# Performance work log

Measured on AMD Instinct MI355X. Metric: run time of the kernel, lower is better.

The kernel has to match this reference:

```python
import jax, jax.numpy as jnp
import numpy as np
import itertools

G = 80          # voxel grid side
N = 200000      # active voxels
A, B = 64, 128  # in/out channels
K = 27          # 3x3x3 kernel offsets
EPS = 1e-5


def _build_kernel_map():
    rng = np.random.default_rng(0)
    flat = rng.choice(G ** 3, size=N, replace=False)
    coords = np.stack(np.unravel_index(flat, (G, G, G)), axis=1).astype(np.int64)  # [N,3]
    lookup = np.full(G ** 3, -1, dtype=np.int64)
    lookup[flat] = np.arange(N)
    gidx = np.full((K, N), N, dtype=np.int32)  # pad with dummy row N
    sidx = np.full((K, N), N, dtype=np.int32)
    for k, off in enumerate(itertools.product([-1, 0, 1], repeat=3)):
        nb = coords + np.asarray(off)
        valid = np.all((nb >= 0) & (nb < G), axis=1)
        i_all = np.nonzero(valid)[0]
        nbf = np.ravel_multi_index(nb[valid].T, (G, G, G))
        j = lookup[nbf]
        m = j >= 0
        i, j = i_all[m], j[m]
        e = len(i)
        gidx[k, :e] = j   # gather neighbor features
        sidx[k, :e] = i   # scatter to output voxel
    return jnp.asarray(gidx), jnp.asarray(sidx)


def setup_inputs() -> dict:
    key = jax.random.key(0)
    ks = jax.random.split(key, 8)
    gidx, sidx = _build_kernel_map()
    return {
        "feats": jax.random.normal(ks[0], (N, A), jnp.float32),
        "w1": jax.random.normal(ks[1], (K, A, B), jnp.float32) * (1.0 / np.sqrt(K * A)),
        "w2": jax.random.normal(ks[2], (K, B, B), jnp.float32) * (1.0 / np.sqrt(K * B)),
        "w_nin": jax.random.normal(ks[3], (A, B), jnp.float32) * (1.0 / np.sqrt(A)),
        "bn1_gamma": jnp.ones((A,), jnp.float32),
        "bn1_beta": jnp.zeros((A,), jnp.float32),
        "bn2_gamma": jnp.ones((B,), jnp.float32),
        "bn2_beta": jnp.zeros((B,), jnp.float32),
        "gidx": gidx,
        "sidx": sidx,
    }


def _bn(x, gamma, beta):
    # MinkowskiBatchNorm: per-channel stats over all active voxels (training mode)
    mean = jnp.mean(x, axis=0)
    var = jnp.var(x, axis=0)
    return (x - mean) * jax.lax.rsqrt(var + EPS) * gamma + beta


def _sparse_conv(feats, w, gidx, sidx):
    # Minkowski sparse conv: for each kernel offset k, gather neighbor feats,
    # apply W[k], scatter-add to output voxel. Dummy row N absorbs padding.
    fp = jnp.concatenate([feats, jnp.zeros((1, feats.shape[1]), feats.dtype)], axis=0)
    out = jnp.zeros((N + 1, w.shape[-1]), feats.dtype)
    for k in range(w.shape[0]):  # fixed 27 offsets
        out = out.at[sidx[k]].add(fp[gidx[k]] @ w[k])
    return out[:N]


def reference(feats, w1, w2, w_nin, bn1_gamma, bn1_beta, bn2_gamma, bn2_beta, gidx, sidx):
    # resblock: BN(a) -> conv3(a->b) -> BN(b) -> conv3(b->b); skip via 1x1 conv (a!=b)
    h = _bn(feats, bn1_gamma, bn1_beta)
    h = _sparse_conv(h, w1, gidx, sidx)
    h = _bn(h, bn2_gamma, bn2_beta)
    residual = _sparse_conv(h, w2, gidx, sidx)
    skip = feats @ w_nin  # kernel_size=1 conv == per-voxel linear
    return skip + residual
```

## Files before the change

kernel.cpp:

```cpp
#include <hip/hip_runtime.h>

#define N_VOX 200000
#define NPAD_INV (27 * N_VOX + 128)
#define EPS_BN 1e-5f

typedef __bf16 bf16x8 __attribute__((ext_vector_type(8)));
typedef float f32x4 __attribute__((ext_vector_type(4)));

__device__ __forceinline__ float bf2f(unsigned short u) {
    union { float f; unsigned int i; } x; x.i = ((unsigned int)u) << 16; return x.f;
}
__device__ __forceinline__ unsigned short f2bf(float f) {
    union { float f; unsigned int i; } x; x.f = f;
    unsigned int r = x.i + 0x7fffu + ((x.i >> 16) & 1u);
    return (unsigned short)(r >> 16);
}

#define ASYNC16(gsrc, ldst)                                                             \
    __builtin_amdgcn_global_load_lds(                                                   \
        (const __attribute__((address_space(1))) void*)(gsrc),                          \
        (__attribute__((address_space(3))) void*)(ldst), 16, 0, 0)

__global__ void fill_inv_kernel(int* __restrict__ inv) {
    for (int i = blockIdx.x * 256 + threadIdx.x; i < NPAD_INV; i += gridDim.x * 256)
        inv[i] = N_VOX;
}

__global__ void build_inv_kernel(const int* __restrict__ sidx, const int* __restrict__ gidx,
                                 int* __restrict__ inv) {
    int k = blockIdx.y;
    int p = blockIdx.x * 256 + threadIdx.x;
    if (p < N_VOX) {
        int s = sidx[k * N_VOX + p];
        if (s < N_VOX) inv[k * N_VOX + s] = gidx[k * N_VOX + p];
    }
}

__global__ void tr_w1_kernel(const float* __restrict__ w, unsigned short* __restrict__ wt) {
    int k = blockIdx.y; int idx = blockIdx.x * 256 + threadIdx.x;
    int a = idx >> 7, b = idx & 127;
    wt[k * 8192 + b * 64 + a] = f2bf(w[k * 8192 + idx]);
}
__global__ void tr_w2_kernel(const float* __restrict__ w, unsigned short* __restrict__ wt) {
    int k = blockIdx.y; int idx = blockIdx.x * 256 + threadIdx.x;
    int a = idx >> 7, b = idx & 127;
    wt[k * 16384 + b * 128 + a] = f2bf(w[k * 16384 + idx]);
}
__global__ void tr_wn_kernel(const float* __restrict__ w, unsigned short* __restrict__ wt) {
    int idx = blockIdx.x * 256 + threadIdx.x;
    int a = idx >> 7, b = idx & 127;
    wt[b * 64 + a] = f2bf(w[idx]);
}

__global__ void stats1_kernel(const float* __restrict__ feats,
                              float* __restrict__ sum, float* __restrict__ sq) {
    int t = threadIdx.x; int c = t & 63; int rg = t >> 6;
    float s = 0.f, q = 0.f;
    for (int row = blockIdx.x * 4 + rg; row < N_VOX; row += gridDim.x * 4) {
        float x = feats[(size_t)row * 64 + c];
        s += x; q += x * x;
    }
    __shared__ float red[8][64];
    red[rg][c] = s; red[4 + rg][c] = q;
    __syncthreads();
    if (t < 64) atomicAdd(&sum[t], red[0][t] + red[1][t] + red[2][t] + red[3][t]);
    else if (t < 128) { int cc = t - 64; atomicAdd(&sq[cc], red[4][cc] + red[5][cc] + red[6][cc] + red[7][cc]); }
}

__global__ void stats2_kernel(const unsigned short* __restrict__ h1b,
                              float* __restrict__ sum, float* __restrict__ sq) {
    int t = threadIdx.x; int c = t & 127; int rg = t >> 7;
    float s = 0.f, q = 0.f;
    for (int row = blockIdx.x * 2 + rg; row < N_VOX; row += gridDim.x * 2) {
        float x = bf2f(h1b[(size_t)row * 128 + c]);
        s += x; q += x * x;
    }
    __shared__ float red[4][128];
    red[rg][c] = s; red[2 + rg][c] = q;
    __syncthreads();
    if (t < 128) atomicAdd(&sum[t], red[0][t] + red[1][t]);
    else { int cc = t - 128; atomicAdd(&sq[cc], red[2][cc] + red[3][cc]); }
}

__global__ void norm1_kernel(const float* __restrict__ feats, const float* __restrict__ ssum,
                             const float* __restrict__ ssq, const float* __restrict__ gamma,
                             const float* __restrict__ beta, unsigned short* __restrict__ fA,
                             unsigned short* __restrict__ fRaw) {
    __shared__ float sc[64], sh[64];
    int t = threadIdx.x;
    if (t < 64) {
        float mean = ssum[t] * (1.0f / N_VOX);
        float var  = ssq[t] * (1.0f / N_VOX) - mean * mean;
        float s    = gamma[t] * rsqrtf(var + EPS_BN);
        sc[t] = s; sh[t] = beta[t] - mean * s;
    }
    __syncthreads();
    const int total = N_VOX * 64 / 8;
    int i = blockIdx.x * 256 + t;
    if (i >= total) return;
    int cb = (i * 8) & 63;
    const float4* src = (const float4*)(feats + (size_t)i * 8);
    float4 f0 = src[0], f1 = src[1];
    float fv[8] = {f0.x, f0.y, f0.z, f0.w, f1.x, f1.y, f1.z, f1.w};
    union { uint4 q; unsigned short u[8]; } a, r;
#pragma unroll
    for (int j = 0; j < 8; j++) {
        a.u[j] = f2bf(fv[j] * sc[cb + j] + sh[cb + j]);
        r.u[j] = f2bf(fv[j]);
    }
    *(uint4*)(fA + (size_t)i * 8) = a.q;
    *(uint4*)(fRaw + (size_t)i * 8) = r.q;
}

__global__ void norm2_kernel(unsigned short* __restrict__ h1b, const float* __restrict__ ssum,
                             const float* __restrict__ ssq, const float* __restrict__ gamma,
                             const float* __restrict__ beta) {
    __shared__ float sc[128], sh[128];
    int t = threadIdx.x;
    if (t < 128) {
        float mean = ssum[t] * (1.0f / N_VOX);
        float var  = ssq[t] * (1.0f / N_VOX) - mean * mean;
        float s    = gamma[t] * rsqrtf(var + EPS_BN);
        sc[t] = s; sh[t] = beta[t] - mean * s;
    }
    __syncthreads();
    const int total = N_VOX * 128 / 8;
    int i = blockIdx.x * 256 + t;
    if (i >= total) return;
    int cb = (i * 8) & 127;
    union { uint4 q; unsigned short u[8]; } v;
    v.q = *(const uint4*)(h1b + (size_t)i * 8);
#pragma unroll
    for (int j = 0; j < 8; j++) v.u[j] = f2bf(bf2f(v.u[j]) * sc[cb + j] + sh[cb + j]);
    *(uint4*)(h1b + (size_t)i * 8) = v.q;
}

__global__ __launch_bounds__(256) void conv1_kernel(
    const unsigned short* __restrict__ fA, const unsigned short* __restrict__ w1t,
    const int* __restrict__ inv, const unsigned short* __restrict__ zp,
    unsigned short* __restrict__ h1b) {
    __shared__ __align__(16) unsigned short sA[2][128 * 64];
    __shared__ __align__(16) unsigned short sB[2][128 * 64];
    const int t = threadIdx.x, lane = t & 63, w = t >> 6;
    const int v0 = blockIdx.x * 128;
    const int srow = w * 32;
    const int lrow = lane >> 3;
    const int lcol = (lane & 7) * 8;
    const int scol = lcol ^ (lrow * 8);
    const int m0 = (w & 1) * 64, n0 = (w >> 1) * 64;
    const int l16 = lane & 15, quad = lane >> 4;
    const int xs = l16 & 7;
    f32x4 acc[4][4] = {};

    auto stage = [&](int k, int b) {
#pragma unroll
        for (int q = 0; q < 4; q++) {
            int rt = srow + q * 8 + lrow;
            int g = inv[k * N_VOX + v0 + rt];
            const unsigned short* asrc = (g < N_VOX) ? (fA + (size_t)g * 64 + scol) : (zp + scol);
            ASYNC16(asrc, &sA[b][(srow + q * 8) * 64]);
            const unsigned short* bsrc = w1t + k * 8192 + rt * 64 + scol;
            ASYNC16(bsrc, &sB[b][(srow + q * 8) * 64]);
        }
    };

    stage(0, 0);
    for (int j = 0; j < 27; j++) {
        const int cb = j & 1;
        if (j + 1 < 27) {
            stage(j + 1, cb ^ 1);
            asm volatile("s_waitcnt vmcnt(8)" ::: "memory");
        } else {
            asm volatile("s_waitcnt vmcnt(0)" ::: "memory");
        }
        __builtin_amdgcn_sched_barrier(0);
        __builtin_amdgcn_s_barrier();
        __builtin_amdgcn_sched_barrier(0);
#pragma unroll
        for (int ks = 0; ks < 2; ks++) {
            const int cs = ((ks * 4 + quad) ^ xs) * 8;
            bf16x8 af[4], bfr[4];
#pragma unroll
            for (int mi = 0; mi < 4; mi++)
                af[mi] = *(const bf16x8*)&sA[cb][(m0 + mi * 16 + l16) * 64 + cs];
#pragma unroll
            for (int ni = 0; ni < 4; ni++)
                bfr[ni] = *(const bf16x8*)&sB[cb][(n0 + ni * 16 + l16) * 64 + cs];
            __builtin_amdgcn_s_setprio(1);
#pragma unroll
            for (int mi = 0; mi < 4; mi++)
#pragma unroll
                for (int ni = 0; ni < 4; ni++)
                    acc[mi][ni] = __builtin_amdgcn_mfma_f32_16x16x32_bf16(af[mi], bfr[ni], acc[mi][ni], 0, 0, 0);
            __builtin_amdgcn_s_setprio(0);
        }
        __builtin_amdgcn_sched_barrier(0);
        __builtin_amdgcn_s_barrier();
        __builtin_amdgcn_sched_barrier(0);
    }
#pragma unroll
    for (int mi = 0; mi < 4; mi++)
#pragma unroll
        for (int r = 0; r < 4; r++) {
            int v = v0 + m0 + mi * 16 + quad * 4 + r;
            if (v < N_VOX) {
#pragma unroll
                for (int ni = 0; ni < 4; ni++)
                    h1b[(size_t)v * 128 + n0 + ni * 16 + l16] = f2bf(acc[mi][ni][r]);
            }
        }
}

__global__ __launch_bounds__(256) void conv2_kernel(
    const unsigned short* __restrict__ h1n, const unsigned short* __restrict__ fRaw,
    const unsigned short* __restrict__ w2t, const unsigned short* __restrict__ w_nint,
    const int* __restrict__ inv, const unsigned short* __restrict__ zp,
    float* __restrict__ out) {
    __shared__ __align__(16) unsigned short sA[2][128 * 64];
    __shared__ __align__(16) unsigned short sB[2][128 * 64];
    const int t = threadIdx.x, lane = t & 63, w = t >> 6;
    const int v0 = blockIdx.x * 128;
    const int srow = w * 32;
    const int lrow = lane >> 3;
    const int lcol = (lane & 7) * 8;
    const int scol = lcol ^ (lrow * 8);
    const int m0 = (w & 1) * 64, n0 = (w >> 1) * 64;
    const int l16 = lane & 15, quad = lane >> 4;
    const int xs = l16 & 7;
    f32x4 acc[4][4] = {};

    auto stage = [&](int j, int b) {
        if (j < 54) {
            const int ko = j >> 1;
            const int kh = (j & 1) * 64;
#pragma unroll
            for (int q = 0; q < 4; q++) {
                int rt = srow + q * 8 + lrow;
                int g = inv[ko * N_VOX + v0 + rt];
                const unsigned short* asrc = (g < N_VOX) ? (h1n + (size_t)g * 128 + kh + scol) : (zp + scol);
                ASYNC16(asrc, &sA[b][(srow + q * 8) * 64]);
                const unsigned short* bsrc = w2t + ko * 16384 + rt * 128 + kh + scol;
                ASYNC16(bsrc, &sB[b][(srow + q * 8) * 64]);
            }
        } else {
#pragma unroll
            for (int q = 0; q < 4; q++) {
                int rt = srow + q * 8 + lrow;
                int v = v0 + rt;
                const unsigned short* asrc = (v < N_VOX) ? (fRaw + (size_t)v * 64 + scol) : (zp + scol);
                ASYNC16(asrc, &sA[b][(srow + q * 8) * 64]);
                const unsigned short* bsrc = w_nint + rt * 64 + scol;
                ASYNC16(bsrc, &sB[b][(srow + q * 8) * 64]);
            }
        }
    };

    stage(0, 0);
    for (int jj = 0; jj < 55; jj++) {
        const int cb = jj & 1;
        if (jj + 1 < 55) {
            stage(jj + 1, cb ^ 1);
            asm volatile("s_waitcnt vmcnt(8)" ::: "memory");
        } else {
            asm volatile("s_waitcnt vmcnt(0)" ::: "memory");
        }
        __builtin_amdgcn_sched_barrier(0);
        __builtin_amdgcn_s_barrier();
        __builtin_amdgcn_sched_barrier(0);
#pragma unroll
        for (int ks = 0; ks < 2; ks++) {
            const int cs = ((ks * 4 + quad) ^ xs) * 8;
            bf16x8 af[4], bfr[4];
#pragma unroll
            for (int mi = 0; mi < 4; mi++)
                af[mi] = *(const bf16x8*)&sA[cb][(m0 + mi * 16 + l16) * 64 + cs];
#pragma unroll
            for (int ni = 0; ni < 4; ni++)
                bfr[ni] = *(const bf16x8*)&sB[cb][(n0 + ni * 16 + l16) * 64 + cs];
            __builtin_amdgcn_s_setprio(1);
#pragma unroll
            for (int mi = 0; mi < 4; mi++)
#pragma unroll
                for (int ni = 0; ni < 4; ni++)
                    acc[mi][ni] = __builtin_amdgcn_mfma_f32_16x16x32_bf16(af[mi], bfr[ni], acc[mi][ni], 0, 0, 0);
            __builtin_amdgcn_s_setprio(0);
        }
        __builtin_amdgcn_sched_barrier(0);
        __builtin_amdgcn_s_barrier();
        __builtin_amdgcn_sched_barrier(0);
    }
#pragma unroll
    for (int mi = 0; mi < 4; mi++)
#pragma unroll
        for (int r = 0; r < 4; r++) {
            int v = v0 + m0 + mi * 16 + quad * 4 + r;
            if (v < N_VOX) {
#pragma unroll
                for (int ni = 0; ni < 4; ni++)
                    out[(size_t)v * 128 + n0 + ni * 16 + l16] = acc[mi][ni][r];
            }
        }
}

extern "C" void kernel_launch(void* const* d_in, const int* in_sizes, int n_in,
                              void* d_out, int out_size, void* d_ws, size_t ws_size,
                              hipStream_t stream) {
    const float* feats = (const float*)d_in[0];
    const float* w1    = (const float*)d_in[1];
    const float* w2    = (const float*)d_in[2];
    const float* w_nin = (const float*)d_in[3];
    const float* g1    = (const float*)d_in[4];
    const float* b1    = (const float*)d_in[5];
    const float* g2    = (const float*)d_in[6];
    const float* b2    = (const float*)d_in[7];
    const int* gidx = (const int*)d_in[8];
    const int* sidx = (const int*)d_in[9];
    float* out = (float*)d_out;

    char* ws = (char*)d_ws;
    int* inv               = (int*)(ws);
    unsigned short* fA     = (unsigned short*)(ws + 21600512);
    unsigned short* fRaw   = (unsigned short*)(ws + 47200512);
    unsigned short* h1b    = (unsigned short*)(ws + 72800512);
    unsigned short* w1t    = (unsigned short*)(ws + 124000512);
    unsigned short* w2t    = (unsigned short*)(ws + 124442880);
    unsigned short* w_nint = (unsigned short*)(ws + 125327616);
    float* stats           = (float*)(ws + 125344000);
    unsigned short* zp     = (unsigned short*)(ws + 125345536);
    float* s1sum = stats, *s1sq = stats + 64, *s2sum = stats + 128, *s2sq = stats + 256;

    hipMemsetAsync(stats, 0, 1536 + 256, stream);
    fill_inv_kernel<<<2048, 256, 0, stream>>>(inv);
    build_inv_kernel<<<dim3(782, 27), 256, 0, stream>>>(sidx, gidx, inv);
    tr_w1_kernel<<<dim3(32, 27), 256, 0, stream>>>(w1, w1t);
    tr_w2_kernel<<<dim3(64, 27), 256, 0, stream>>>(w2, w2t);
    tr_wn_kernel<<<32, 256, 0, stream>>>(w_nin, w_nint);
    stats1_kernel<<<512, 256, 0, stream>>>(feats, s1sum, s1sq);
    norm1_kernel<<<6250, 256, 0, stream>>>(feats, s1sum, s1sq, g1, b1, fA, fRaw);
    conv1_kernel<<<1563, 256, 0, stream>>>(fA, w1t, inv, zp, h1b);
    stats2_kernel<<<512, 256, 0, stream>>>(h1b, s2sum, s2sq);
    norm2_kernel<<<12500, 256, 0, stream>>>(h1b, s2sum, s2sq, g2, b2);
    conv2_kernel<<<1563, 256, 0, stream>>>(h1b, fRaw, w2t, w_nint, inv, zp, out);
}
```

Before: 757.1 us.

## Fold batch-norm affine into conv weights and fuse stats into conv epilogue

Batch-norm scale is folded into the transposed conv weights, and the shift becomes a per-offset bias term. That bias is added per output row only for the kernel offsets that have a valid neighbor, tracked with a shared-memory presence bitmask. This removes the separate normalize passes over the activations and the fA buffer. The second BN's statistics are accumulated in the conv1 epilogue, and the raw-feature conversion, input stats and inv fill are merged into a single prep kernel. The trade-off is extra atomics and bias work in the conv kernels, and slightly different bf16 rounding because the scale is applied to the weights instead of the activations.

Measured after the change: 1.345 ms. +77.7%, slower.

```diff
diff --git a/kernel.cpp b/kernel.cpp
--- a/kernel.cpp
+++ b/kernel.cpp
@@ -21,9 +21,49 @@
         (const __attribute__((address_space(1))) void*)(gsrc),                          \
         (__attribute__((address_space(3))) void*)(ldst), 16, 0, 0)
 
-__global__ void fill_inv_kernel(int* __restrict__ inv) {
-    for (int i = blockIdx.x * 256 + threadIdx.x; i < NPAD_INV; i += gridDim.x * 256)
-        inv[i] = N_VOX;
+__global__ void prep0_kernel(const float* __restrict__ feats, const float* __restrict__ w_nin,
+                             int* __restrict__ inv, unsigned short* __restrict__ w_nint,
+                             unsigned short* __restrict__ fRaw,
+                             float* __restrict__ s1sum, float* __restrict__ s1sq) {
+    __shared__ float rs[64], rq[64];
+    const int t = threadIdx.x;
+    if (t < 64) { rs[t] = 0.f; rq[t] = 0.f; }
+    __syncthreads();
+    const int stride = gridDim.x * 256;
+    for (int i = blockIdx.x * 256 + t; i < NPAD_INV; i += stride) inv[i] = N_VOX;
+    for (int i = blockIdx.x * 256 + t; i < 8192; i += stride) {
+        int a = i >> 7, b = i & 127;
+        w_nint[b * 64 + a] = f2bf(w_nin[i]);
+    }
+    float s[8] = {}, q[8] = {};
+    const int total = N_VOX * 64 / 8;
+    for (int i = blockIdx.x * 256 + t; i < total; i += stride) {
+        const float4* src = (const float4*)(feats + (size_t)i * 8);
+        float4 f0 = src[0], f1 = src[1];
+        float fv[8] = {f0.x, f0.y, f0.z, f0.w, f1.x, f1.y, f1.z, f1.w};
+        union { uint4 u4; unsigned short u[8]; } r;
+#pragma unroll
+        for (int j = 0; j < 8; j++) {
+            r.u[j] = f2bf(fv[j]);
+            s[j] += fv[j]; q[j] += fv[j] * fv[j];
+        }
+        *(uint4*)(fRaw + (size_t)i * 8) = r.u4;
+    }
+#pragma unroll
+    for (int j = 0; j < 8; j++) {
+        s[j] += __shfl_xor(s[j], 8, 64); s[j] += __shfl_xor(s[j], 16, 64); s[j] += __shfl_xor(s[j], 32, 64);
+        q[j] += __shfl_xor(q[j], 8, 64); q[j] += __shfl_xor(q[j], 16, 64); q[j] += __shfl_xor(q[j], 32, 64);
+    }
+    const int lane = t & 63;
+    if (lane < 8) {
+#pragma unroll
+        for (int j = 0; j < 8; j++) {
+            atomicAdd(&rs[lane * 8 + j], s[j]);
+            atomicAdd(&rq[lane * 8 + j], q[j]);
+        }
+    }
+    __syncthreads();
+    if (t < 64) { atomicAdd(&s1sum[t], rs[t]); atomicAdd(&s1sq[t], rq[t]); }
 }
 
 __global__ void build_inv_kernel(const int* __restrict__ sidx, const int* __restrict__ gidx,
@@ -36,111 +76,71 @@
     }
 }
 
-__global__ void tr_w1_kernel(const float* __restrict__ w, unsigned short* __restrict__ wt) {
-    int k = blockIdx.y; int idx = blockIdx.x * 256 + threadIdx.x;
-    int a = idx >> 7, b = idx & 127;
-    wt[k * 8192 + b * 64 + a] = f2bf(w[k * 8192 + idx]);
-}
-__global__ void tr_w2_kernel(const float* __restrict__ w, unsigned short* __restrict__ wt) {
-    int k = blockIdx.y; int idx = blockIdx.x * 256 + threadIdx.x;
-    int a = idx >> 7, b = idx & 127;
-    wt[k * 16384 + b * 128 + a] = f2bf(w[k * 16384 + idx]);
-}
-__global__ void tr_wn_kernel(const float* __restrict__ w, unsigned short* __restrict__ wt) {
-    int idx = blockIdx.x * 256 + threadIdx.x;
-    int a = idx >> 7, b = idx & 127;
-    wt[b * 64 + a] = f2bf(w[idx]);
-}
-
-__global__ void stats1_kernel(const float* __restrict__ feats,
-                              float* __restrict__ sum, float* __restrict__ sq) {
-    int t = threadIdx.x; int c = t & 63; int rg = t >> 6;
-    float s = 0.f, q = 0.f;
-    for (int row = blockIdx.x * 4 + rg; row < N_VOX; row += gridDim.x * 4) {
-        float x = feats[(size_t)row * 64 + c];
-        s += x; q += x * x;
-    }
-    __shared__ float red[8][64];
-    red[rg][c] = s; red[4 + rg][c] = q;
-    __syncthreads();
-    if (t < 64) atomicAdd(&sum[t], red[0][t] + red[1][t] + red[2][t] + red[3][t]);
-    else if (t < 128) { int cc = t - 64; atomicAdd(&sq[cc], red[4][cc] + red[5][cc] + red[6][cc] + red[7][cc]); }
-}
-
-__global__ void stats2_kernel(const unsigned short* __restrict__ h1b,
-                              float* __restrict__ sum, float* __restrict__ sq) {
-    int t = threadIdx.x; int c = t & 127; int rg = t >> 7;
-    float s = 0.f, q = 0.f;
-    for (int row = blockIdx.x * 2 + rg; row < N_VOX; row += gridDim.x * 2) {
-        float x = bf2f(h1b[(size_t)row * 128 + c]);
-        s += x; q += x * x;
-    }
-    __shared__ float red[4][128];
-    red[rg][c] = s; red[2 + rg][c] = q;
-    __syncthreads();
-    if (t < 128) atomicAdd(&sum[t], red[0][t] + red[1][t]);
-    else { int cc = t - 128; atomicAdd(&sq[cc], red[2][cc] + red[3][cc]); }
-}
-
-__global__ void norm1_kernel(const float* __restrict__ feats, const float* __restrict__ ssum,
-                             const float* __restrict__ ssq, const float* __restrict__ gamma,
-                             const float* __restrict__ beta, unsigned short* __restrict__ fA,
-                             unsigned short* __restrict__ fRaw) {
-    __shared__ float sc[64], sh[64];
-    int t = threadIdx.x;
+__global__ void prep1_kernel(const float* __restrict__ w1, const float* __restrict__ s1sum,
+                             const float* __restrict__ s1sq, const float* __restrict__ g1,
+                             const float* __restrict__ b1, unsigned short* __restrict__ w1t,
+                             float* __restrict__ T1g) {
+    __shared__ float lsc[64], lsh[64];
+    const int t = threadIdx.x;
     if (t < 64) {
-        float mean = ssum[t] * (1.0f / N_VOX);
-        float var  = ssq[t] * (1.0f / N_VOX) - mean * mean;
-        float s    = gamma[t] * rsqrtf(var + EPS_BN);
-        sc[t] = s; sh[t] = beta[t] - mean * s;
-    }
-    __syncthreads();
-    const int total = N_VOX * 64 / 8;
-    int i = blockIdx.x * 256 + t;
-    if (i >= total) return;
-    int cb = (i * 8) & 63;
-    const float4* src = (const float4*)(feats + (size_t)i * 8);
-    float4 f0 = src[0], f1 = src[1];
-    float fv[8] = {f0.x, f0.y, f0.z, f0.w, f1.x, f1.y, f1.z, f1.w};
-    union { uint4 q; unsigned short u[8]; } a, r;
-#pragma unroll
-    for (int j = 0; j < 8; j++) {
-        a.u[j] = f2bf(fv[j] * sc[cb + j] + sh[cb + j]);
-        r.u[j] = f2bf(fv[j]);
-    }
-    *(uint4*)(fA + (size_t)i * 8) = a.q;
-    *(uint4*)(fRaw + (size_t)i * 8) = r.q;
-}
-
-__global__ void norm2_kernel(unsigned short* __restrict__ h1b, const float* __restrict__ ssum,
-                             const float* __restrict__ ssq, const float* __restrict__ gamma,
-                             const float* __restrict__ beta) {
-    __shared__ float sc[128], sh[128];
-    int t = threadIdx.x;
+        float mean = s1sum[t] * (1.0f / N_VOX);
+        float var  = s1sq[t] * (1.0f / N_VOX) - mean * mean;
+        float sc   = g1[t] * rsqrtf(var + EPS_BN);
+        lsc[t] = sc; lsh[t] = b1[t] - mean * sc;
+    }
+    __syncthreads();
+    const int stride = gridDim.x * 256;
+    for (int e = blockIdx.x * 256 + t; e < 27 * 8192; e += stride) {
+        int k = e >> 13, idx = e & 8191;
+        int a = idx >> 7, n = idx & 127;
+        w1t[k * 8192 + n * 64 + a] = f2bf(w1[e] * lsc[a]);
+    }
+    int o = blockIdx.x * 256 + t;
+    if (o < 27 * 128) {
+        int k = o >> 7, n = o & 127;
+        float sacc = 0.f;
+        for (int a = 0; a < 64; a++) sacc += lsh[a] * w1[k * 8192 + a * 128 + n];
+        T1g[o] = sacc;
+    }
+}
+
+__global__ void prep2_kernel(const float* __restrict__ w2, const float* __restrict__ s2sum,
+                             const float* __restrict__ s2sq, const float* __restrict__ g2,
+                             const float* __restrict__ b2, unsigned short* __restrict__ w2t,
+                             float* __restrict__ T2g) {
+    __shared__ float lsc[128], lsh[128];
+    const int t = threadIdx.x;
     if (t < 128) {
-        float mean = ssum[t] * (1.0f / N_VOX);
-        float var  = ssq[t] * (1.0f / N_VOX) - mean * mean;
-        float s    = gamma[t] * rsqrtf(var + EPS_BN);
-        sc[t] = s; sh[t] = beta[t] - mean * s;
-    }
-    __syncthreads();
-    const int total = N_VOX * 128 / 8;
-    int i = blockIdx.x * 256 + t;
-    if (i >= total) return;
-    int cb = (i * 8) & 127;
-    union { uint4 q; unsigned short u[8]; } v;
-    v.q = *(const uint4*)(h1b + (size_t)i * 8);
-#pragma unroll
-    for (int j = 0; j < 8; j++) v.u[j] = f2bf(bf2f(v.u[j]) * sc[cb + j] + sh[cb + j]);
-    *(uint4*)(h1b + (size_t)i * 8) = v.q;
+        float mean = s2sum[t] * (1.0f / N_VOX);
+        float var  = s2sq[t] * (1.0f / N_VOX) - mean * mean;
+        float sc   = g2[t] * rsqrtf(var + EPS_BN);
+        lsc[t] = sc; lsh[t] = b2[t] - mean * sc;
+    }
+    __syncthreads();
+    const int stride = gridDim.x * 256;
+    for (int e = blockIdx.x * 256 + t; e < 27 * 16384; e += stride) {
+        int k = e >> 14, idx = e & 16383;
+        int a = idx >> 7, n = idx & 127;
+        w2t[k * 16384 + n * 128 + a] = f2bf(w2[e] * lsc[a]);
+    }
+    int o = blockIdx.x * 256 + t;
+    if (o < 27 * 128) {
+        int k = o >> 7, n = o & 127;
+        float sacc = 0.f;
+        for (int a = 0; a < 128; a++) sacc += lsh[a] * w2[k * 16384 + a * 128 + n];
+        T2g[o] = sacc;
+    }
 }
 
 __global__ __launch_bounds__(256) void conv1_kernel(
-    const unsigned short* __restrict__ fA, const unsigned short* __restrict__ w1t,
+    const unsigned short* __restrict__ fRaw, const unsigned short* __restrict__ w1t,
     const int* __restrict__ inv, const unsigned short* __restrict__ zp,
-    unsigned short* __restrict__ h1b) {
+    const float* __restrict__ T1g, unsigned short* __restrict__ h1b,
+    float* __restrict__ s2sum, float* __restrict__ s2sq) {
     __shared__ __align__(16) unsigned short sA[2][128 * 64];
     __shared__ __align__(16) unsigned short sB[2][128 * 64];
+    __shared__ unsigned int presmask[128];
+    __shared__ float s2s[128], s2q[128];
     const int t = threadIdx.x, lane = t & 63, w = t >> 6;
     const int v0 = blockIdx.x * 128;
     const int srow = w * 32;
@@ -152,12 +152,16 @@
     const int xs = l16 & 7;
     f32x4 acc[4][4] = {};
 
+    if (t < 128) { presmask[t] = 0u; s2s[t] = 0.f; s2q[t] = 0.f; }
+    __syncthreads();
+
     auto stage = [&](int k, int b) {
 #pragma unroll
         for (int q = 0; q < 4; q++) {
             int rt = srow + q * 8 + lrow;
             int g = inv[k * N_VOX + v0 + rt];
-            const unsigned short* asrc = (g < N_VOX) ? (fA + (size_t)g * 64 + scol) : (zp + scol);
+            if ((lane & 7) == 0 && g < N_VOX) atomicOr(&presmask[rt], 1u << k);
+            const unsigned short* asrc = (g < N_VOX) ? (fRaw + (size_t)g * 64 + scol) : (zp + scol);
             ASYNC16(asrc, &sA[b][(srow + q * 8) * 64]);
             const unsigned short* bsrc = w1t + k * 8192 + rt * 64 + scol;
             ASYNC16(bsrc, &sB[b][(srow + q * 8) * 64]);
@@ -198,6 +202,32 @@
         __builtin_amdgcn_s_barrier();
         __builtin_amdgcn_sched_barrier(0);
     }
+
+    float* Tl = (float*)&sA[0][0];
+    for (int idx = t; idx < 27 * 128; idx += 256) Tl[idx] = T1g[idx];
+    __syncthreads();
+
+    unsigned int rm[16];
+#pragma unroll
+    for (int mi = 0; mi < 4; mi++)
+#pragma unroll
+        for (int r = 0; r < 4; r++)
+            rm[mi * 4 + r] = presmask[m0 + mi * 16 + quad * 4 + r];
+    for (int k = 0; k < 27; k++) {
+        float tk0 = Tl[k * 128 + n0 + l16];
+        float tk1 = Tl[k * 128 + n0 + 16 + l16];
+        float tk2 = Tl[k * 128 + n0 + 32 + l16];
+        float tk3 = Tl[k * 128 + n0 + 48 + l16];
+#pragma unroll
+        for (int mi = 0; mi < 4; mi++)
+#pragma unroll
+            for (int r = 0; r < 4; r++)
+                if ((rm[mi * 4 + r] >> k) & 1u) {
+                    acc[mi][0][r] += tk0; acc[mi][1][r] += tk1;
+                    acc[mi][2][r] += tk2; acc[mi][3][r] += tk3;
+                }
+    }
+    float ps[4] = {}, pq[4] = {};
 #pragma unroll
     for (int mi = 0; mi < 4; mi++)
 #pragma unroll
@@ -205,19 +235,37 @@
             int v = v0 + m0 + mi * 16 + quad * 4 + r;
             if (v < N_VOX) {
 #pragma unroll
-                for (int ni = 0; ni < 4; ni++)
-                    h1b[(size_t)v * 128 + n0 + ni * 16 + l16] = f2bf(acc[mi][ni][r]);
+                for (int ni = 0; ni < 4; ni++) {
+                    float x = acc[mi][ni][r];
+                    ps[ni] += x; pq[ni] += x * x;
+                    h1b[(size_t)v * 128 + n0 + ni * 16 + l16] = f2bf(x);
+                }
             }
         }
+#pragma unroll
+    for (int ni = 0; ni < 4; ni++) {
+        ps[ni] += __shfl_xor(ps[ni], 16, 64); ps[ni] += __shfl_xor(ps[ni], 32, 64);
+        pq[ni] += __shfl_xor(pq[ni], 16, 64); pq[ni] += __shfl_xor(pq[ni], 32, 64);
+    }
+    if (lane < 16) {
+#pragma unroll
+        for (int ni = 0; ni < 4; ni++) {
+            atomicAdd(&s2s[n0 + ni * 16 + lane], ps[ni]);
+            atomicAdd(&s2q[n0 + ni * 16 + lane], pq[ni]);
+        }
+    }
+    __syncthreads();
+    if (t < 128) { atomicAdd(&s2sum[t], s2s[t]); atomicAdd(&s2sq[t], s2q[t]); }
 }
 
 __global__ __launch_bounds__(256) void conv2_kernel(
     const unsigned short* __restrict__ h1n, const unsigned short* __restrict__ fRaw,
     const unsigned short* __restrict__ w2t, const unsigned short* __restrict__ w_nint,
     const int* __restrict__ inv, const unsigned short* __restrict__ zp,
-    float* __restrict__ out) {
+    const float* __restrict__ T2g, float* __restrict__ out) {
     __shared__ __align__(16) unsigned short sA[2][128 * 64];
     __shared__ __align__(16) unsigned short sB[2][128 * 64];
+    __shared__ unsigned int presmask[128];
     const int t = threadIdx.x, lane = t & 63, w = t >> 6;
     const int v0 = blockIdx.x * 128;
     const int srow = w * 32;
@@ -229,6 +277,9 @@
     const int xs = l16 & 7;
     f32x4 acc[4][4] = {};
 
+    if (t < 128) presmask[t] = 0u;
+    __syncthreads();
+
     auto stage = [&](int j, int b) {
         if (j < 54) {
             const int ko = j >> 1;
@@ -237,6 +288,7 @@
             for (int q = 0; q < 4; q++) {
                 int rt = srow + q * 8 + lrow;
                 int g = inv[ko * N_VOX + v0 + rt];
+                if ((j & 1) == 0 && (lane & 7) == 0 && g < N_VOX) atomicOr(&presmask[rt], 1u << ko);
                 const unsigned short* asrc = (g < N_VOX) ? (h1n + (size_t)g * 128 + kh + scol) : (zp + scol);
                 ASYNC16(asrc, &sA[b][(srow + q * 8) * 64]);
                 const unsigned short* bsrc = w2t + ko * 16384 + rt * 128 + kh + scol;
@@ -288,6 +340,31 @@
         __builtin_amdgcn_sched_barrier(0);
         __builtin_amdgcn_s_barrier();
         __builtin_amdgcn_sched_barrier(0);
+    }
+
+    float* Tl = (float*)&sA[0][0];
+    for (int idx = t; idx < 27 * 128; idx += 256) Tl[idx] = T2g[idx];
+    __syncthreads();
+
+    unsigned int rm[16];
+#pragma unroll
+    for (int mi = 0; mi < 4; mi++)
+#pragma unroll
+        for (int r = 0; r < 4; r++)
+            rm[mi * 4 + r] = presmask[m0 + mi * 16 + quad * 4 + r];
+    for (int k = 0; k < 27; k++) {
+        float tk0 = Tl[k * 128 + n0 + l16];
+        float tk1 = Tl[k * 128 + n0 + 16 + l16];
+        float tk2 = Tl[k * 128 + n0 + 32 + l16];
+        float tk3 = Tl[k * 128 + n0 + 48 + l16];
+#pragma unroll
+        for (int mi = 0; mi < 4; mi++)
+#pragma unroll
+            for (int r = 0; r < 4; r++)
+                if ((rm[mi * 4 + r] >> k) & 1u) {
+                    acc[mi][0][r] += tk0; acc[mi][1][r] += tk1;
+                    acc[mi][2][r] += tk2; acc[mi][3][r] += tk3;
+                }
     }
 #pragma unroll
     for (int mi = 0; mi < 4; mi++)
@@ -319,26 +396,22 @@
 
     char* ws = (char*)d_ws;
     int* inv               = (int*)(ws);
-    unsigned short* fA     = (unsigned short*)(ws + 21600512);
-    unsigned short* fRaw   = (unsigned short*)(ws + 47200512);
-    unsigned short* h1b    = (unsigned short*)(ws + 72800512);
-    unsigned short* w1t    = (unsigned short*)(ws + 124000512);
-    unsigned short* w2t    = (unsigned short*)(ws + 124442880);
-    unsigned short* w_nint = (unsigned short*)(ws + 125327616);
-    float* stats           = (float*)(ws + 125344000);
-    unsigned short* zp     = (unsigned short*)(ws + 125345536);
+    unsigned short* fRaw   = (unsigned short*)(ws + 21600512);
+    unsigned short* h1b    = (unsigned short*)(ws + 47200512);
+    unsigned short* w1t    = (unsigned short*)(ws + 98400512);
+    unsigned short* w2t    = (unsigned short*)(ws + 98842880);
+    unsigned short* w_nint = (unsigned short*)(ws + 99727616);
+    float* T1g             = (float*)(ws + 99744000);
+    float* T2g             = (float*)(ws + 99757824);
+    float* stats           = (float*)(ws + 99771648);
+    unsigned short* zp     = (unsigned short*)(ws + 99773184);
     float* s1sum = stats, *s1sq = stats + 64, *s2sum = stats + 128, *s2sq = stats + 256;
 
     hipMemsetAsync(stats, 0, 1536 + 256, stream);
-    fill_inv_kernel<<<2048, 256, 0, stream>>>(inv);
+    prep0_kernel<<<1024, 256, 0, stream>>>(feats, w_nin, inv, w_nint, fRaw, s1sum, s1sq);
     build_inv_kernel<<<dim3(782, 27), 256, 0, stream>>>(sidx, gidx, inv);
-    tr_w1_kernel<<<dim3(32, 27), 256, 0, stream>>>(w1, w1t);
-    tr_w2_kernel<<<dim3(64, 27), 256, 0, stream>>>(w2, w2t);
-    tr_wn_kernel<<<32, 256, 0, stream>>>(w_nin, w_nint);
-    stats1_kernel<<<512, 256, 0, stream>>>(feats, s1sum, s1sq);
-    norm1_kernel<<<6250, 256, 0, stream>>>(feats, s1sum, s1sq, g1, b1, fA, fRaw);
-    conv1_kernel<<<1563, 256, 0, stream>>>(fA, w1t, inv, zp, h1b);
-    stats2_kernel<<<512, 256, 0, stream>>>(h1b, s2sum, s2sq);
-    norm2_kernel<<<12500, 256, 0, stream>>>(h1b, s2sum, s2sq, g2, b2);
-    conv2_kernel<<<1563, 256, 0, stream>>>(h1b, fRaw, w2t, w_nint, inv, zp, out);
-}
+    prep1_kernel<<<512, 256, 0, stream>>>(w1, s1sum, s1sq, g1, b1, w1t, T1g);
+    conv1_kernel<<<1563, 256, 0, stream>>>(fRaw, w1t, inv, zp, T1g, h1b, s2sum, s2sq);
+    prep2_kernel<<<512, 256, 0, stream>>>(w2, s2sum, s2sq, g2, b2, w2t, T2g);
+    conv2_kernel<<<1563, 256, 0, stream>>>(h1b, fRaw, w2t, w_nint, inv, zp, T2g, out);
+}
```
